# Optimization experiments

Hardware: AMD Instinct MI355X
Metric: run time of the kernel (lower is better)

The kernel has to match this reference:

```python
import jax, jax.numpy as jnp
import numpy as np

HIDDEN = 768
MLP = 4 * HIDDEN

def layernorm(x, g, b, eps=1e-5):
    mu = jnp.mean(x, axis=-1, keepdims=True)
    var = jnp.var(x, axis=-1, keepdims=True)
    return (x - mu) * jax.lax.rsqrt(var + eps) * g + b

def setup_inputs() -> dict:
    key = jax.random.key(0)
    ks = jax.random.split(key, 10)
    b, l, h = 8, 1024, HIDDEN
    s = 1.0 / np.sqrt(h)
    inp = {
        "x": jax.random.normal(ks[0], (b, l, h), dtype=jnp.float32),
        "Wq": jax.random.normal(ks[1], (h, h), dtype=jnp.float32) * s,
        "Wk": jax.random.normal(ks[2], (h, h), dtype=jnp.float32) * s,
        "Wv": jax.random.normal(ks[3], (h, h), dtype=jnp.float32) * s,
        "Wo": jax.random.normal(ks[4], (h, h), dtype=jnp.float32) * s,
        "W1": jax.random.normal(ks[5], (h, MLP), dtype=jnp.float32) * s,
        "b1": jnp.zeros((MLP,), dtype=jnp.float32),
        "W2": jax.random.normal(ks[6], (MLP, h), dtype=jnp.float32) * (1.0 / np.sqrt(MLP)),
        "b2": jnp.zeros((h,), dtype=jnp.float32),
        "g1": jnp.ones((h,), dtype=jnp.float32),
        "be1": jnp.zeros((h,), dtype=jnp.float32),
        "g2": jnp.ones((h,), dtype=jnp.float32),
        "be2": jnp.zeros((h,), dtype=jnp.float32),
        "n_heads": 12,
    }
    return inp

def reference(x, Wq, Wk, Wv, Wo, W1, b1, W2, b2, g1, be1, g2, be2, n_heads):
    b, l, h = x.shape
    d = h // n_heads
    # NOTE: faithful to source — heads are the LAST axis of a plain reshape,
    # and the second einsum contracts with K (not V), reproducing the original code.
    q = (x @ Wq).reshape(b, l, d, n_heads)
    k = (x @ Wk).reshape(b, l, d, n_heads)
    v = (x @ Wv).reshape(b, l, d, n_heads)  # computed but unused downstream, as in source
    scores = jnp.einsum('bldn,bmdn->blmn', q, k) / (d ** 0.5)
    attn = jax.nn.softmax(scores, axis=2)  # softmax over m (dim=2), as in source
    ctx = jnp.einsum('blmn,bmdn->bldn', attn, k).reshape(b, l, h)
    attn_out = ctx @ Wo
    x = x + attn_out
    x = layernorm(x, g1, be1)
    ff = (jax.nn.gelu(x @ W1 + b1, approximate=False) @ W2) + b2
    x = x + ff
    x = layernorm(x, g2, be2)
    return x
```

## Files before the change

kernel.cpp:

```cpp
#include <hip/hip_runtime.h>
#include <math.h>

typedef unsigned short u16;
typedef unsigned int u32;
typedef short bf16x8 __attribute__((ext_vector_type(8)));
typedef float f32x4 __attribute__((ext_vector_type(4)));

#define MFMA(a, b, c) __builtin_amdgcn_mfma_f32_16x16x32_bf16((a), (b), (c), 0, 0, 0)

#define GLOAD_LDS16(g, l)                                                              \
    __builtin_amdgcn_global_load_lds((const __attribute__((address_space(1))) void*)(g), \
                                     (__attribute__((address_space(3))) void*)(l), 16, 0, 0)

__device__ __forceinline__ u16 f2bf(float f) {
    u32 u = __float_as_uint(f);
    u32 r = (u + 0x7fffu + ((u >> 16) & 1u)) >> 16;
    return (u16)r;
}

__device__ __forceinline__ u16 f2bf_trunc(float f) {
    return (u16)(__float_as_uint(f) >> 16);
}

__device__ __forceinline__ float fast_gelu(float z) {
    float u = fminf(1.5957691216f * z * (1.0f + 0.044715f * z * z), 80.0f);
    float e = __expf(u);
    float r = __builtin_amdgcn_rcpf(e + 1.0f);
    return z * e * r;
}

__device__ void dev_xcast(const float* __restrict__ in, u16* __restrict__ out, int blk) {
    size_t i = ((size_t)blk * 256 + threadIdx.x) * 8;
    const float4* p = reinterpret_cast<const float4*>(in + i);
    float4 a = p[0], b = p[1];
    union { u16 u[8]; uint4 v; } o;
    o.u[0] = f2bf(a.x); o.u[1] = f2bf(a.y); o.u[2] = f2bf(a.z); o.u[3] = f2bf(a.w);
    o.u[4] = f2bf(b.x); o.u[5] = f2bf(b.y); o.u[6] = f2bf(b.z); o.u[7] = f2bf(b.w);
    *reinterpret_cast<uint4*>(out + i) = o.v;
}

__device__ void dev_transpose(const float* __restrict__ in, u16* __restrict__ out,
                              int K, int N, int bx, int by, float* tile ) {
    int k0 = by * 64, n0 = bx * 64;
    int t = threadIdx.x;
    for (int p = 0; p < 16; p++) {
        int idx = t + p * 256;
        int r = idx >> 6, c = idx & 63;
        tile[r * 65 + c] = in[(size_t)(k0 + r) * N + n0 + c];
    }
    __syncthreads();
    for (int p = 0; p < 16; p++) {
        int idx = t + p * 256;
        int nr = idx >> 6, nc = idx & 63;
        out[(size_t)(n0 + nr) * K + k0 + nc] = f2bf(tile[nc * 65 + nr]);
    }
}

__device__ void dev_wo(const float* __restrict__ in, u16* __restrict__ out,
                       int bx, int by, float* tile ) {
    int k0 = by * 96, n0 = bx * 64;
    int t = threadIdx.x;
    for (int p = 0; p < 24; p++) {
        int idx = t + p * 256;
        int r = idx >> 6, c = idx & 63;
        tile[r * 65 + c] = in[(size_t)(k0 + r) * 768 + n0 + c];
    }
    __syncthreads();
    for (int p = 0; p < 3; p++) {
        int idx = t + p * 256;
        int c = idx / 12, n = idx % 12;
        union { u16 u[8]; uint4 v; } o;
        for (int j = 0; j < 8; j++) o.u[j] = f2bf(tile[(j * 12 + n) * 65 + c]);
        *reinterpret_cast<uint4*>(&out[(size_t)(n0 + c) * 768 + n * 64 + by * 8]) = o.v;
    }
}

__global__ __launch_bounds__(256) void prep_k(const float* __restrict__ x,
                                              const float* __restrict__ Wq,
                                              const float* __restrict__ Wk,
                                              const float* __restrict__ Wo,
                                              const float* __restrict__ W1,
                                              const float* __restrict__ W2,
                                              u16* __restrict__ XB,
                                              u16* __restrict__ WQKT,
                                              u16* __restrict__ WOT,
                                              u16* __restrict__ W1T,
                                              u16* __restrict__ W2T) {
    __shared__ float tile[96 * 65];
    int bid = blockIdx.x;
    if (bid < 3072) {
        dev_xcast(x, XB, bid);
    } else if (bid < 3216) {
        int b = bid - 3072; dev_transpose(Wq, WQKT, 768, 768, b % 12, b / 12, tile);
    } else if (bid < 3360) {
        int b = bid - 3216; dev_transpose(Wk, WQKT + (size_t)768 * 768, 768, 768, b % 12, b / 12, tile);
    } else if (bid < 3456) {
        int b = bid - 3360; dev_wo(Wo, WOT, b % 12, b / 12, tile);
    } else if (bid < 4032) {
        int b = bid - 3456; dev_transpose(W1, W1T, 768, 3072, b % 48, b / 48, tile);
    } else {
        int b = bid - 4032; dev_transpose(W2, W2T, 3072, 768, b % 12, b / 12, tile);
    }
}

__global__ __launch_bounds__(256) void head_pack_k(const u16* __restrict__ in, int ld,
                                                   u16* __restrict__ out,
                                                   u16* __restrict__ outT) {
    __shared__ u16 tile[16 * 768];
    int b = blockIdx.y;
    int l0 = blockIdx.x * 16;
    int t = threadIdx.x;
    for (int p = 0; p < 6; p++) {
        int c = t + p * 256;
        int li = c / 96, dc = c % 96;
        *reinterpret_cast<uint4*>(&tile[li * 768 + dc * 8]) =
            *reinterpret_cast<const uint4*>(&in[(size_t)(b * 1024 + l0 + li) * ld + dc * 8]);
    }
    __syncthreads();
    for (int p = 0; p < 6; p++) {
        int c = t + p * 256;
        int n = c >> 7, rem = c & 127, li = rem >> 3, k8 = rem & 7;
        union { u16 u[8]; uint4 v; } o;
        for (int j = 0; j < 8; j++) o.u[j] = tile[li * 768 + (k8 * 8 + j) * 12 + n];
        *reinterpret_cast<uint4*>(&out[(size_t)((b * 12 + n) * 1024 + l0 + li) * 64 + k8 * 8]) = o.v;
    }
    for (int p = 0; p < 6; p++) {
        int c = t + p * 256;
        int n = c >> 7;
        int rem = c & 127;
        int d = rem >> 1;
        int half = rem & 1;
        union { u16 u[8]; uint4 v; } o;
        for (int j = 0; j < 8; j++) o.u[j] = tile[(half * 8 + j) * 768 + d * 12 + n];
        *reinterpret_cast<uint4*>(
            &outT[((size_t)(b * 12 + n) * 64 + d) * 1024 + l0 + half * 8]) = o.v;
    }
}

template <int EPI, int TM, bool AH = false, int NSO = 0, bool KSPLIT = false>
__global__ __launch_bounds__(256) void gemm_bt_k(const u16* __restrict__ A,
                                                 const u16* __restrict__ BT,
                                                 int M, int N, int K, int NBX,
                                                 float* __restrict__ outF,
                                                 u16* __restrict__ outB,
                                                 const float* __restrict__ resid,
                                                 const float* __restrict__ bias) {
    constexpr int MI = TM / 32;
    constexpr int NS = NSO ? NSO : ((TM == 64) ? 4 : 3);
    constexpr int LPS = (TM == 128) ? 4 : 3;
    constexpr int VC = LPS * (NS - 2);
    __shared__ __align__(16) u16 As[NS][TM * 32];
    __shared__ __align__(16) u16 Bs[NS][128 * 32];

    int L = blockIdx.x;
    int kp = 0;
    if constexpr (KSPLIT) {
        int half = gridDim.x >> 1;
        if (L >= half) { kp = 1; L -= half; }
    }
    int bx = (L >> 3) % NBX;
    int by = (L / (8 * NBX)) * 8 + (L & 7);
    int m0 = by * TM, n0 = bx * 128;

    int t = threadIdx.x;
    int wave = t >> 6, lane = t & 63;
    int wr = (wave >> 1) * (TM / 2), wc = (wave & 1) * 64;
    int ln = lane & 15, quad = lane >> 4;
    int sw = quad ^ ((ln >> 1) & 3);

    int e0 = t, e1 = t + 256;
    int r0 = e0 >> 2, c0 = (e0 & 3) ^ ((r0 >> 1) & 3);
    int r1 = e1 >> 2, c1 = (e1 & 3) ^ ((r1 >> 1) & 3);
    int kofs = 0;
    if constexpr (KSPLIT) kofs = kp * (K >> 1);
    int ahk = 0;
    if constexpr (KSPLIT && AH) ahk = kp * (K >> 4);
    const u16* A0 = A + (size_t)(m0 + r0) * K + kofs + c0 * 8;
    const u16* A1 = A + (size_t)(m0 + r1) * K + kofs + c1 * 8;
    const u16* B0 = BT + (size_t)(n0 + r0) * K + kofs + c0 * 8;
    const u16* B1 = BT + (size_t)(n0 + r1) * K + kofs + c1 * 8;
    const u16* Abase = nullptr;
    if constexpr (AH) {
        int m = m0 + r0;
        Abase = A + ((size_t)(m >> 10) * 12288 + (m & 1023)) * 64;
    }

    int nk = K >> 5;
    if constexpr (KSPLIT) nk >>= 1;

    f32x4 acc[MI][4];
    for (int i = 0; i < MI; i++)
        for (int j = 0; j < 4; j++)
            for (int r = 0; r < 4; r++) acc[i][j][r] = 0.0f;

    for (int s = 0; s < NS - 1; s++) {
        if constexpr (AH) {
            int col8 = ahk + s * 4 + c0;
            GLOAD_LDS16(Abase + (col8 >> 3) * 65536 + (col8 & 7) * 8, &As[s][e0 * 8]);
        } else {
            GLOAD_LDS16(A0 + s * 32, &As[s][e0 * 8]);
            if constexpr (TM == 128) GLOAD_LDS16(A1 + s * 32, &As[s][e1 * 8]);
        }
        GLOAD_LDS16(B0 + s * 32, &Bs[s][e0 * 8]);
        GLOAD_LDS16(B1 + s * 32, &Bs[s][e1 * 8]);
    }

    for (int kb = 0; kb < nk; kb += NS) {
#pragma unroll
        for (int s = 0; s < NS; s++) {
            int k = kb + s;
            if constexpr (VC == 6)      asm volatile("s_waitcnt vmcnt(6)" ::: "memory");
            else if constexpr (VC == 4) asm volatile("s_waitcnt vmcnt(4)" ::: "memory");
            else if constexpr (VC == 3) asm volatile("s_waitcnt vmcnt(3)" ::: "memory");
            else                        asm volatile("s_waitcnt vmcnt(0)" ::: "memory");
            asm volatile("s_barrier" ::: "memory");
            {
                int ks = k + NS - 1 < nk ? k + NS - 1 : nk - 1;
                int stage = (s + NS - 1) % NS;
                if constexpr (AH) {
                    int col8 = ahk + ks * 4 + c0;
                    GLOAD_LDS16(Abase + (col8 >> 3) * 65536 + (col8 & 7) * 8, &As[stage][e0 * 8]);
                } else {
                    GLOAD_LDS16(A0 + ks * 32, &As[stage][e0 * 8]);
                    if constexpr (TM == 128) GLOAD_LDS16(A1 + ks * 32, &As[stage][e1 * 8]);
                }
                GLOAD_LDS16(B0 + ks * 32, &Bs[stage][e0 * 8]);
                GLOAD_LDS16(B1 + ks * 32, &Bs[stage][e1 * 8]);
            }
            const u16* as = As[s];
            const u16* bs = Bs[s];
            bf16x8 afr[MI], bfr[4];
            for (int i = 0; i < MI; i++)
                afr[i] = *reinterpret_cast<const bf16x8*>(&as[(wr + i * 16 + ln) * 32 + sw * 8]);
            for (int j = 0; j < 4; j++)
                bfr[j] = *reinterpret_cast<const bf16x8*>(&bs[(wc + j * 16 + ln) * 32 + sw * 8]);
            for (int i = 0; i < MI; i++)
                for (int j = 0; j < 4; j++)
                    acc[i][j] = MFMA(afr[i], bfr[j], acc[i][j]);
        }
    }

    for (int i = 0; i < MI; i++) {
        for (int j = 0; j < 4; j++) {
            int col = n0 + wc + j * 16 + ln;
            for (int r = 0; r < 4; r++) {
                int row = m0 + wr + i * 16 + quad * 4 + r;
                size_t idx = (size_t)row * N + col;
                float v = acc[i][j][r];
                if constexpr (EPI == 1) {
                    if constexpr (KSPLIT) {
                        if (kp == 0) outF[idx] = resid[idx] + v;
                        else reinterpret_cast<float*>(outB)[idx] = v;
                    } else {
                        outF[idx] = resid[idx] + v;
                    }
                } else if constexpr (EPI == 2) {
                    outB[idx] = f2bf(fast_gelu(v + bias[col]));
                } else if constexpr (EPI == 3) {
                    if constexpr (KSPLIT) {
                        if (kp == 0) outF[idx] = resid[idx] + v + bias[col];
                        else reinterpret_cast<float*>(outB)[idx] = v;
                    } else {
                        outF[idx] = resid[idx] + v + bias[col];
                    }
                } else {
                    outB[idx] = f2bf(col < 768 ? v * 0.18033688011112042f : v);
                }
            }
        }
    }
}

__global__ __launch_bounds__(256) void attention_k(const u16* __restrict__ QB, int ldq,
                                                   const u16* __restrict__ KH,
                                                   const u16* __restrict__ KHT,
                                                   u16* __restrict__ CTXH) {
    __shared__ __align__(16) u16 Ks[64 * 72];
    __shared__ __align__(16) u16 KsT[64 * 72];
    __shared__ __align__(16) u16 Pl[4][16 * 72];
    int bh = blockIdx.y;
    int b = bh / 12, n = bh % 12;
    int l0 = blockIdx.x * 64;
    int t = threadIdx.x, wave = t >> 6, lane = t & 63;
    int ln = lane & 15, quad = lane >> 4;
    int lw = l0 + wave * 16;

    bf16x8 a0, a1;
    {
        union { u16 u[8]; bf16x8 v; } q0, q1;
        const u16* qrow = QB + (size_t)(b * 1024 + lw + ln) * ldq + n;
        for (int j = 0; j < 8; j++) {
            q0.u[j] = qrow[(quad * 8 + j) * 12];
            q1.u[j] = qrow[(32 + quad * 8 + j) * 12];
        }
        a0 = q0.v; a1 = q1.v;
    }

    f32x4 o[4];
    for (int dt = 0; dt < 4; dt++)
        for (int r = 0; r < 4; r++) o[dt][r] = 0.0f;
    float lst[4];
    for (int r = 0; r < 4; r++) lst[r] = 0.0f;

    const u16* Kbase  = KH  + (size_t)bh * 65536;
    const u16* KTbase = KHT + (size_t)bh * 65536;
    int mi = t & 63, ds = (t >> 6) * 16;

    uint4 kva = *reinterpret_cast<const uint4*>(&Kbase[(size_t)mi * 64 + ds]);
    uint4 kvb = *reinterpret_cast<const uint4*>(&Kbase[(size_t)mi * 64 + ds + 8]);
    uint4 kta = *reinterpret_cast<const uint4*>(&KTbase[(size_t)mi * 1024 + ds]);
    uint4 ktb = *reinterpret_cast<const uint4*>(&KTbase[(size_t)mi * 1024 + ds + 8]);

    for (int mb = 0; mb < 16; mb++) {
        __syncthreads();
        *reinterpret_cast<uint4*>(&Ks[mi * 72 + ds]) = kva;
        *reinterpret_cast<uint4*>(&Ks[mi * 72 + ds + 8]) = kvb;
        *reinterpret_cast<uint4*>(&KsT[mi * 72 + ds]) = kta;
        *reinterpret_cast<uint4*>(&KsT[mi * 72 + ds + 8]) = ktb;
        __syncthreads();

        {
            int mnext = (mb + 1 < 16 ? mb + 1 : 15) * 64;
            kva = *reinterpret_cast<const uint4*>(&Kbase[(size_t)(mnext + mi) * 64 + ds]);
            kvb = *reinterpret_cast<const uint4*>(&Kbase[(size_t)(mnext + mi) * 64 + ds + 8]);
            kta = *reinterpret_cast<const uint4*>(&KTbase[(size_t)mi * 1024 + mnext + ds]);
            ktb = *reinterpret_cast<const uint4*>(&KTbase[(size_t)mi * 1024 + mnext + ds + 8]);
        }

        f32x4 st[4];
        for (int nt = 0; nt < 4; nt++) {
            bf16x8 bk0 = *reinterpret_cast<bf16x8*>(&Ks[(nt * 16 + ln) * 72 + quad * 8]);
            bf16x8 bk1 = *reinterpret_cast<bf16x8*>(&Ks[(nt * 16 + ln) * 72 + 32 + quad * 8]);
            f32x4 z;
            for (int r = 0; r < 4; r++) z[r] = 0.0f;
            z = MFMA(a0, bk0, z);
            st[nt] = MFMA(a1, bk1, z);
        }

        for (int r = 0; r < 4; r++) {
            int row = quad * 4 + r;
            float psum = 0.0f;
            for (int nt = 0; nt < 4; nt++) {
                float p = exp2f(st[nt][r]);
                psum += p;
                Pl[wave][row * 72 + nt * 16 + ln] = f2bf_trunc(p);
            }
            lst[r] += psum;
        }

        bf16x8 pf0 = *reinterpret_cast<bf16x8*>(&Pl[wave][ln * 72 + quad * 8]);
        bf16x8 pf1 = *reinterpret_cast<bf16x8*>(&Pl[wave][ln * 72 + 32 + quad * 8]);
        for (int dt = 0; dt < 4; dt++) {
            bf16x8 bk0 = *reinterpret_cast<bf16x8*>(&KsT[(dt * 16 + ln) * 72 + quad * 8]);
            bf16x8 bk1 = *reinterpret_cast<bf16x8*>(&KsT[(dt * 16 + ln) * 72 + 32 + quad * 8]);
            o[dt] = MFMA(pf0, bk0, o[dt]);
            o[dt] = MFMA(pf1, bk1, o[dt]);
        }
    }

    for (int r = 0; r < 4; r++)
        for (int off = 1; off < 16; off <<= 1) lst[r] += __shfl_xor(lst[r], off, 64);

    u16* out = CTXH + (size_t)bh * 65536;
    for (int r = 0; r < 4; r++) {
        float inv = 1.0f / lst[r];
        int row = lw + quad * 4 + r;
        for (int dt = 0; dt < 4; dt++)
            out[(size_t)row * 64 + dt * 16 + ln] = f2bf(o[dt][r] * inv);
    }
}

__global__ __launch_bounds__(256) void layernorm_k(const float* __restrict__ in,
                                                   float* __restrict__ outF,
                                                   u16* __restrict__ outB,
                                                   const float* __restrict__ g,
                                                   const float* __restrict__ be,
                                                   const float* __restrict__ in2) {
    __shared__ float red[8];
    int row = blockIdx.x;
    int t = threadIdx.x;
    const float* p = in + (size_t)row * 768;
    float v0 = p[t], v1 = p[t + 256], v2 = p[t + 512];
    if (in2) {
        const float* p2 = in2 + (size_t)row * 768;
        v0 += p2[t]; v1 += p2[t + 256]; v2 += p2[t + 512];
    }
    float s = v0 + v1 + v2;
    float ss = v0 * v0 + v1 * v1 + v2 * v2;
    for (int off = 32; off >= 1; off >>= 1) {
        s += __shfl_xor(s, off, 64);
        ss += __shfl_xor(ss, off, 64);
    }
    int wave = t >> 6, lane = t & 63;
    if (lane == 0) { red[wave] = s; red[4 + wave] = ss; }
    __syncthreads();
    float S = red[0] + red[1] + red[2] + red[3];
    float SS = red[4] + red[5] + red[6] + red[7];
    float mean = S * (1.0f / 768.0f);
    float var = SS * (1.0f / 768.0f) - mean * mean;
    float rstd = rsqrtf(var + 1e-5f);
    float o0 = (v0 - mean) * rstd * g[t] + be[t];
    float o1 = (v1 - mean) * rstd * g[t + 256] + be[t + 256];
    float o2 = (v2 - mean) * rstd * g[t + 512] + be[t + 512];
    float* q = outF + (size_t)row * 768;
    q[t] = o0; q[t + 256] = o1; q[t + 512] = o2;
    if (outB) {
        u16* qb = outB + (size_t)row * 768;
        qb[t] = f2bf(o0); qb[t + 256] = f2bf(o1); qb[t + 512] = f2bf(o2);
    }
}

extern "C" void kernel_launch(void* const* d_in, const int* in_sizes, int n_in,
                              void* d_out, int out_size, void* d_ws, size_t ws_size,
                              hipStream_t stream) {
    const float* x   = (const float*)d_in[0];
    const float* Wq  = (const float*)d_in[1];
    const float* Wk  = (const float*)d_in[2];
    const float* Wo  = (const float*)d_in[4];
    const float* W1  = (const float*)d_in[5];
    const float* b1  = (const float*)d_in[6];
    const float* W2  = (const float*)d_in[7];
    const float* b2  = (const float*)d_in[8];
    const float* g1  = (const float*)d_in[9];
    const float* be1 = (const float*)d_in[10];
    const float* g2  = (const float*)d_in[11];
    const float* be2 = (const float*)d_in[12];
    float* out = (float*)d_out;

    const int S = 8192, H = 768, MLP4 = 3072, H2 = 1536;

    char* ws = (char*)d_ws;
    u16* XB   = (u16*)ws;  ws += (size_t)S * H * 2;
    u16* WQKT = (u16*)ws;  ws += (size_t)H2 * H * 2;
    u16* WOT  = (u16*)ws;  ws += (size_t)H * H * 2;
    u16* W1T  = (u16*)ws;  ws += (size_t)H * MLP4 * 2;
    u16* W2T  = (u16*)ws;  ws += (size_t)H * MLP4 * 2;
    u16* QKB  = (u16*)ws;  ws += (size_t)S * H2 * 2;
    u16* KH   = (u16*)ws;  ws += (size_t)S * H * 2;
    float* Y  = (float*)ws; ws += (size_t)S * H * 4;
    u16* HB   = (u16*)ws;  ws += (size_t)S * MLP4 * 2;

    u16* CTXH = XB;
    u16* X1B  = QKB;
    u16* KHT  = HB;
    float* Y1 = (float*)QKB;

    prep_k<<<4608, 256, 0, stream>>>(x, Wq, Wk, Wo, W1, W2, XB, WQKT, WOT, W1T, W2T);

    gemm_bt_k<4, 128><<<12 * 64, 256, 0, stream>>>(XB, WQKT, S, H2, H, 12, nullptr, QKB, nullptr, nullptr);

    head_pack_k<<<dim3(64, 8), 256, 0, stream>>>(QKB + H, H2, KH, KHT);
    attention_k<<<dim3(16, 96), 256, 0, stream>>>(QKB, H2, KH, KHT, CTXH);

    gemm_bt_k<1, 64, true><<<6 * 128, 256, 0, stream>>>(CTXH, WOT, S, H, H, 6, Y, nullptr, x, nullptr);
    layernorm_k<<<S, 256, 0, stream>>>(Y, Y, X1B, g1, be1, nullptr);

    gemm_bt_k<2, 128><<<24 * 64, 256, 0, stream>>>(X1B, W1T, S, MLP4, H, 24, nullptr, HB, nullptr, b1);
    gemm_bt_k<3, 128, false, 0, true><<<2 * 6 * 64, 256, 0, stream>>>(HB, W2T, S, H, MLP4, 6, Y, (u16*)Y1, Y, b2);
    layernorm_k<<<S, 256, 0, stream>>>(Y, out, nullptr, g2, be2, Y1);
}
```

Before: 411.3 us.

## Use 512-thread GEMM blocks for QK/W1 and drop K-split in W2 GEMM

Adds a thread-count template parameter so the 128x128 GEMM tile can run with 8 waves (2x4 wave grid, each handling 64x32), halving per-thread loads and accumulators. The QK and W1 projections now launch with 512 threads. The W2 GEMM drops the K-split (and its second partial buffer added in layernorm) in favour of a 64-row tile with 256 threads. This trades per-wave MFMA reuse for more waves to hide latency, and removes the split-K partial write/read at the cost of fewer blocks for the W2 GEMM.

```diff
diff --git a/kernel.cpp b/kernel.cpp
--- a/kernel.cpp
+++ b/kernel.cpp
@@ -137,17 +137,21 @@
     }
 }
 
-template <int EPI, int TM, bool AH = false, int NSO = 0, bool KSPLIT = false>
-__global__ __launch_bounds__(256) void gemm_bt_k(const u16* __restrict__ A,
-                                                 const u16* __restrict__ BT,
-                                                 int M, int N, int K, int NBX,
-                                                 float* __restrict__ outF,
-                                                 u16* __restrict__ outB,
-                                                 const float* __restrict__ resid,
-                                                 const float* __restrict__ bias) {
-    constexpr int MI = TM / 32;
+template <int EPI, int TM, bool AH = false, int NSO = 0, bool KSPLIT = false, int NT = 256>
+__global__ __launch_bounds__(NT) void gemm_bt_k(const u16* __restrict__ A,
+                                                const u16* __restrict__ BT,
+                                                int M, int N, int K, int NBX,
+                                                float* __restrict__ outF,
+                                                u16* __restrict__ outB,
+                                                const float* __restrict__ resid,
+                                                const float* __restrict__ bias) {
     constexpr int NS = NSO ? NSO : ((TM == 64) ? 4 : 3);
-    constexpr int LPS = (TM == 128) ? 4 : 3;
+    constexpr int WN = (NT == 512) ? 4 : 2;
+    constexpr int MI = (TM / 2) / 16;
+    constexpr int NJ = (128 / WN) / 16;
+    constexpr int ALD = (TM == 128 && NT == 256) ? 2 : 1;
+    constexpr int BLD = (NT == 256) ? 2 : 1;
+    constexpr int LPS = ALD + BLD;
     constexpr int VC = LPS * (NS - 2);
     __shared__ __align__(16) u16 As[NS][TM * 32];
     __shared__ __align__(16) u16 Bs[NS][128 * 32];
@@ -164,7 +168,7 @@
 
     int t = threadIdx.x;
     int wave = t >> 6, lane = t & 63;
-    int wr = (wave >> 1) * (TM / 2), wc = (wave & 1) * 64;
+    int wr = (wave / WN) * (TM / 2), wc = (wave % WN) * (128 / WN);
     int ln = lane & 15, quad = lane >> 4;
     int sw = quad ^ ((ln >> 1) & 3);
 
@@ -188,9 +192,9 @@
     int nk = K >> 5;
     if constexpr (KSPLIT) nk >>= 1;
 
-    f32x4 acc[MI][4];
+    f32x4 acc[MI][NJ];
     for (int i = 0; i < MI; i++)
-        for (int j = 0; j < 4; j++)
+        for (int j = 0; j < NJ; j++)
             for (int r = 0; r < 4; r++) acc[i][j][r] = 0.0f;
 
     for (int s = 0; s < NS - 1; s++) {
@@ -199,10 +203,10 @@
             GLOAD_LDS16(Abase + (col8 >> 3) * 65536 + (col8 & 7) * 8, &As[s][e0 * 8]);
         } else {
             GLOAD_LDS16(A0 + s * 32, &As[s][e0 * 8]);
-            if constexpr (TM == 128) GLOAD_LDS16(A1 + s * 32, &As[s][e1 * 8]);
+            if constexpr (ALD == 2) GLOAD_LDS16(A1 + s * 32, &As[s][e1 * 8]);
         }
         GLOAD_LDS16(B0 + s * 32, &Bs[s][e0 * 8]);
-        GLOAD_LDS16(B1 + s * 32, &Bs[s][e1 * 8]);
+        if constexpr (BLD == 2) GLOAD_LDS16(B1 + s * 32, &Bs[s][e1 * 8]);
     }
 
     for (int kb = 0; kb < nk; kb += NS) {
@@ -212,6 +216,7 @@
             if constexpr (VC == 6)      asm volatile("s_waitcnt vmcnt(6)" ::: "memory");
             else if constexpr (VC == 4) asm volatile("s_waitcnt vmcnt(4)" ::: "memory");
             else if constexpr (VC == 3) asm volatile("s_waitcnt vmcnt(3)" ::: "memory");
+            else if constexpr (VC == 2) asm volatile("s_waitcnt vmcnt(2)" ::: "memory");
             else                        asm volatile("s_waitcnt vmcnt(0)" ::: "memory");
             asm volatile("s_barrier" ::: "memory");
             {
@@ -222,26 +227,26 @@
                     GLOAD_LDS16(Abase + (col8 >> 3) * 65536 + (col8 & 7) * 8, &As[stage][e0 * 8]);
                 } else {
                     GLOAD_LDS16(A0 + ks * 32, &As[stage][e0 * 8]);
-                    if constexpr (TM == 128) GLOAD_LDS16(A1 + ks * 32, &As[stage][e1 * 8]);
+                    if constexpr (ALD == 2) GLOAD_LDS16(A1 + ks * 32, &As[stage][e1 * 8]);
                 }
                 GLOAD_LDS16(B0 + ks * 32, &Bs[stage][e0 * 8]);
-                GLOAD_LDS16(B1 + ks * 32, &Bs[stage][e1 * 8]);
+                if constexpr (BLD == 2) GLOAD_LDS16(B1 + ks * 32, &Bs[stage][e1 * 8]);
             }
             const u16* as = As[s];
             const u16* bs = Bs[s];
-            bf16x8 afr[MI], bfr[4];
+            bf16x8 afr[MI], bfr[NJ];
             for (int i = 0; i < MI; i++)
                 afr[i] = *reinterpret_cast<const bf16x8*>(&as[(wr + i * 16 + ln) * 32 + sw * 8]);
-            for (int j = 0; j < 4; j++)
+            for (int j = 0; j < NJ; j++)
                 bfr[j] = *reinterpret_cast<const bf16x8*>(&bs[(wc + j * 16 + ln) * 32 + sw * 8]);
             for (int i = 0; i < MI; i++)
-                for (int j = 0; j < 4; j++)
+                for (int j = 0; j < NJ; j++)
                     acc[i][j] = MFMA(afr[i], bfr[j], acc[i][j]);
         }
     }
 
     for (int i = 0; i < MI; i++) {
-        for (int j = 0; j < 4; j++) {
+        for (int j = 0; j < NJ; j++) {
             int col = n0 + wc + j * 16 + ln;
             for (int r = 0; r < 4; r++) {
                 int row = m0 + wr + i * 16 + quad * 4 + r;
@@ -443,11 +448,10 @@
     u16* CTXH = XB;
     u16* X1B  = QKB;
     u16* KHT  = HB;
-    float* Y1 = (float*)QKB;
 
     prep_k<<<4608, 256, 0, stream>>>(x, Wq, Wk, Wo, W1, W2, XB, WQKT, WOT, W1T, W2T);
 
-    gemm_bt_k<4, 128><<<12 * 64, 256, 0, stream>>>(XB, WQKT, S, H2, H, 12, nullptr, QKB, nullptr, nullptr);
+    gemm_bt_k<4, 128, false, 0, false, 512><<<12 * 64, 512, 0, stream>>>(XB, WQKT, S, H2, H, 12, nullptr, QKB, nullptr, nullptr);
 
     head_pack_k<<<dim3(64, 8), 256, 0, stream>>>(QKB + H, H2, KH, KHT);
     attention_k<<<dim3(16, 96), 256, 0, stream>>>(QKB, H2, KH, KHT, CTXH);
@@ -455,7 +459,7 @@
     gemm_bt_k<1, 64, true><<<6 * 128, 256, 0, stream>>>(CTXH, WOT, S, H, H, 6, Y, nullptr, x, nullptr);
     layernorm_k<<<S, 256, 0, stream>>>(Y, Y, X1B, g1, be1, nullptr);
 
-    gemm_bt_k<2, 128><<<24 * 64, 256, 0, stream>>>(X1B, W1T, S, MLP4, H, 24, nullptr, HB, nullptr, b1);
-    gemm_bt_k<3, 128, false, 0, true><<<2 * 6 * 64, 256, 0, stream>>>(HB, W2T, S, H, MLP4, 6, Y, (u16*)Y1, Y, b2);
-    layernorm_k<<<S, 256, 0, stream>>>(Y, out, nullptr, g2, be2, Y1);
-}
+    gemm_bt_k<2, 128, false, 0, false, 512><<<24 * 64, 512, 0, stream>>>(X1B, W1T, S, MLP4, H, 24, nullptr, HB, nullptr, b1);
+    gemm_bt_k<3, 64><<<6 * 128, 256, 0, stream>>>(HB, W2T, S, H, MLP4, 6, Y, nullptr, Y, b2);
+    layernorm_k<<<S, 256, 0, stream>>>(Y, out, nullptr, g2, be2, nullptr);
+}
```

New measurement: 395.9 us. 3.8% less time.
